# Performance work log

Measured on AMD Instinct MI355X. Metric: run time of the kernel, lower is better.

The kernel has to match this reference:

```python
import jax, jax.numpy as jnp
import numpy as np

B, C_IN, H, W = 4, 1536, 64, 64   # SGI input: cat of three 512-ch encoder maps at 64x64
HID, OUT = 1536, 512
N = H * W


def _grid_edge_index(h, w):
    # 4-connected bidirectional grid, matching SGI.grid_edge_index
    idx = np.arange(h * w).reshape(h, w)
    right = np.stack([idx[:, :-1].ravel(), idx[:, 1:].ravel()])
    down = np.stack([idx[:-1, :].ravel(), idx[1:, :].ravel()])
    ei = np.concatenate([right, down, right[::-1], down[::-1]], axis=1)
    return ei.astype(np.int32)


def setup_inputs() -> dict:
    key = jax.random.key(0)
    ks = jax.random.split(key, 7)
    ei = _grid_edge_index(H, W)
    s = 0.02
    return {
        "x":  jax.random.normal(ks[0], (B, C_IN, H, W), jnp.float32),
        "W1": jax.random.normal(ks[1], (C_IN, HID), jnp.float32) * s,
        "b1": jnp.zeros((HID,), jnp.float32),
        "W2": jax.random.normal(ks[2], (HID, OUT), jnp.float32) * s,
        "b2": jnp.zeros((OUT,), jnp.float32),
        "Wl": jax.random.normal(ks[3], (C_IN, OUT), jnp.float32) * s,
        "bl": jnp.zeros((OUT,), jnp.float32),
        "src": jnp.asarray(ei[0]),
        "dst": jnp.asarray(ei[1]),
    }


def _gcn(h_in, Wt, b, src, dst, inv_sqrt_deg, inv_deg):
    # PyG GCNConv: lin -> symmetric-normalized aggregation (with self loops) -> +bias
    h = h_in @ Wt                                   # [B, N, F]
    norm = inv_sqrt_deg[src] * inv_sqrt_deg[dst]    # [E]
    msgs = h[:, src, :] * norm[None, :, None]       # [B, E, F]
    # self-loop contribution has norm 1/deg_i
    agg = (h * inv_deg[None, :, None]).at[:, dst, :].add(msgs)
    return agg + b


def reference(x, W1, b1, W2, b2, Wl, bl, src, dst):
    Bb, C, Hh, Ww = x.shape
    n = Hh * Ww
    # degree including self loop (graph is symmetric)
    deg = jnp.zeros((n,), x.dtype).at[dst].add(1.0) + 1.0
    inv_sqrt_deg = jax.lax.rsqrt(deg)
    inv_deg = 1.0 / deg

    xt = x.reshape(Bb, C, n).transpose(0, 2, 1)     # [B, N, C]
    identity = xt
    origin = xt @ Wl + bl                           # [B, N, OUT]
    h = jax.nn.relu(_gcn(xt, W1, b1, src, dst, inv_sqrt_deg, inv_deg))
    h = _gcn(h + identity, W2, b2, src, dst, inv_sqrt_deg, inv_deg)
    out = h * origin                                # [B, N, OUT]
    return out.transpose(0, 2, 1).reshape(Bb, out.shape[-1], Hh, Ww)
```

## Files before the change

### kernel.cpp

```cpp
#include <hip/hip_runtime.h>
#include <hip/hip_bf16.h>
#include <stdint.h>


typedef __bf16 bf16;
typedef float f32x4 __attribute__((ext_vector_type(4)));
typedef bf16 bf16x8 __attribute__((ext_vector_type(8)));

#define NB 4
#define NN 4096
#define CIN 1536
#define HIDF 1536
#define OUTF 512

__device__ __forceinline__ float degree_of(int n) {
  const int x = n & 63, y = n >> 6;
  return 1.0f + (x > 0) + (x < 63) + (y > 0) + (y < 63);
}
__device__ __forceinline__ float deg2(int gx, int gy) {
  return 1.0f + (gx > 0) + (gx < 63) + (gy > 0) + (gy < 63);
}

#define XBLK 6144
#define W1BLK 576
#define W2BLK 192

__global__ __launch_bounds__(256) void prep(
    const float* __restrict__ x, const float* __restrict__ W1,
    const float* __restrict__ W2, const float* __restrict__ Wl,
    bf16* __restrict__ xt, bf16* __restrict__ xa, bf16* __restrict__ w1t,
    bf16* __restrict__ w2t, bf16* __restrict__ wlt) {
  __shared__ float vt[64 * 64];
  __shared__ float at[64 * 64];
  const int B = blockIdx.x, t = threadIdx.x;
  const int tx = t & 15, ty = t >> 4;
  const int lane = t & 63, w = t >> 6;
  const int u = lane & 7, n3 = lane >> 3;

  if (B < XBLK) {
    const int slot = B >> 3;
    const int nt = (B & 7) * 8 + (slot & 7);
    const int ct = (slot >> 3) % 24;
    const int bb = (slot >> 3) / 24;
    const int gy = nt;
    const int n0 = nt * 64, c0 = ct * 64;
    const float* xb = x + (long)bb * CIN * NN;
#pragma unroll
    for (int cc = 0; cc < 4; cc++) {
      const int cl = ty * 4 + cc;
      const float* row = xb + (long)(c0 + cl) * NN + n0;
      const int nb = tx * 4;
      f32x4 v = *(const f32x4*)(row + nb);
      f32x4 up = {0.f, 0.f, 0.f, 0.f};
      f32x4 dn = {0.f, 0.f, 0.f, 0.f};
      if (gy > 0) up = *(const f32x4*)(row + nb - 64);
      if (gy < 63) dn = *(const f32x4*)(row + nb + 64);
      const float lf = (tx > 0) ? row[nb - 1] : 0.f;
      const float rt = (tx < 15) ? row[nb + 4] : 0.f;
      f32x4 a;
#pragma unroll
      for (int i = 0; i < 4; i++) {
        const int gx = nb + i;
        const float degn = deg2(gx, gy);
        float s = v[i] * (1.0f / degn);
        const float lv = (i == 0) ? lf : v[i - 1];
        const float rv = (i == 3) ? rt : v[i + 1];
        if (gx > 0) s += lv * rsqrtf(degn * deg2(gx - 1, gy));
        if (gx < 63) s += rv * rsqrtf(degn * deg2(gx + 1, gy));
        if (gy > 0) s += up[i] * rsqrtf(degn * deg2(gx, gy - 1));
        if (gy < 63) s += dn[i] * rsqrtf(degn * deg2(gx, gy + 1));
        a[i] = s;
      }
      const int chunk = tx ^ (2 * ((cl >> 3) & 7));
      *(f32x4*)&vt[cl * 64 + chunk * 4] = v;
      *(f32x4*)&at[cl * 64 + chunk * 4] = a;
    }
    __syncthreads();
    bf16* xtb = xt + (long)bb * NN * CIN;
    bf16* xab = xa + (long)bb * NN * CIN;
#pragma unroll
    for (int q = 0; q < 4; q++) {
      const int j = q * 4 + w;
      const int arr = j & 1, r = j >> 1;
      const int nl = n3 + 8 * r;
      const float* s = arr ? at : vt;
      bf16x8 o;
#pragma unroll
      for (int jj = 0; jj < 8; jj++) {
        const int cl = u * 8 + jj;
        const int col = nl ^ (8 * ((cl >> 3) & 7));
        o[jj] = (bf16)s[cl * 64 + col];
      }
      bf16* outp = arr ? xab : xtb;
      *(bf16x8*)&outp[(long)(n0 + nl) * CIN + c0 + u * 8] = o;
    }
  } else {
    int B2 = B - XBLK;
    const float* srcp;
    bf16* dstp;
    int Fdim, Kd, nt, ct;
    if (B2 < W1BLK) {
      nt = B2 / 24; ct = B2 % 24; srcp = W1; dstp = w1t; Fdim = HIDF; Kd = CIN;
    } else if (B2 < W1BLK + W2BLK) {
      const int l = B2 - W1BLK;
      nt = l / 24; ct = l % 24; srcp = W2; dstp = w2t; Fdim = OUTF; Kd = HIDF;
    } else {
      const int l = B2 - W1BLK - W2BLK;
      nt = l / 24; ct = l % 24; srcp = Wl; dstp = wlt; Fdim = OUTF; Kd = CIN;
    }
    const int n0 = nt * 64, c0 = ct * 64;
#pragma unroll
    for (int cc = 0; cc < 4; cc++) {
      const int cl = ty * 4 + cc;
      const float* row = srcp + (long)(c0 + cl) * Fdim + n0;
      f32x4 v = *(const f32x4*)(row + tx * 4);
      const int chunk = tx ^ (2 * ((cl >> 3) & 7));
      *(f32x4*)&vt[cl * 64 + chunk * 4] = v;
    }
    __syncthreads();
#pragma unroll
    for (int q = 0; q < 2; q++) {
      const int r = q * 4 + w;
      const int nl = n3 + 8 * r;
      bf16x8 o;
#pragma unroll
      for (int jj = 0; jj < 8; jj++) {
        const int cl = u * 8 + jj;
        const int col = nl ^ (8 * ((cl >> 3) & 7));
        o[jj] = (bf16)vt[cl * 64 + col];
      }
      *(bf16x8*)&dstp[(long)(n0 + nl) * Kd + c0 + u * 8] = o;
    }
  }
}

__device__ __forceinline__ void async_copy16(const void* g, void* l) {
  __builtin_amdgcn_global_load_lds(
      (const __attribute__((address_space(1))) void*)g,
      (__attribute__((address_space(3))) void*)l, 16, 0, 0);
}

struct GemmCtx {
  f32x4 acc[4][4];
  int wave, lane, wm, wn, quad, l15;
};

__device__ __forceinline__ void gemm_init(GemmCtx& cx, int t) {
  cx.wave = t >> 6;
  cx.lane = t & 63;
  cx.wm = (cx.wave & 1) * 64;
  cx.wn = (cx.wave >> 1) * 64;
  cx.quad = cx.lane >> 4;
  cx.l15 = cx.lane & 15;
#pragma unroll
  for (int i = 0; i < 4; i++)
#pragma unroll
    for (int j = 0; j < 4; j++) cx.acc[i][j] = {0.f, 0.f, 0.f, 0.f};
}

template <int K>
__device__ __forceinline__ void gemm_kloop(GemmCtx& cx, const bf16* Ab,
                                           const bf16* Bb, bf16* As,
                                           bf16* Bs) {
  const int r = cx.lane >> 3, c8 = cx.lane & 7;
  const int fchunk = c8 ^ r;
  for (int kt = 0; kt < K; kt += 64) {
#pragma unroll
    for (int i = 0; i < 4; i++) {
      const int row = i * 32 + cx.wave * 8;
      async_copy16(Ab + (long)(row + r) * K + kt + fchunk * 8, &As[row * 64]);
      async_copy16(Bb + (long)(row + r) * K + kt + fchunk * 8, &Bs[row * 64]);
    }
    __syncthreads();
#pragma unroll
    for (int kk = 0; kk < 2; kk++) {
      const int q = kk * 4 + cx.quad;
      bf16x8 af[4], bfv[4];
#pragma unroll
      for (int mr = 0; mr < 4; mr++) {
        const int m = cx.wm + mr * 16 + cx.l15;
        af[mr] = *(const bf16x8*)&As[m * 64 + (q ^ (m & 7)) * 8];
      }
#pragma unroll
      for (int nc = 0; nc < 4; nc++) {
        const int n = cx.wn + nc * 16 + cx.l15;
        bfv[nc] = *(const bf16x8*)&Bs[n * 64 + (q ^ (n & 7)) * 8];
      }
#pragma unroll
      for (int mr = 0; mr < 4; mr++)
#pragma unroll
        for (int nc = 0; nc < 4; nc++)
          cx.acc[mr][nc] = __builtin_amdgcn_mfma_f32_16x16x32_bf16(
              af[mr], bfv[nc], cx.acc[mr][nc], 0, 0, 0);
    }
    __syncthreads();
  }
}

__global__ __launch_bounds__(256) void gemm_h(
    const bf16* __restrict__ xa, const bf16* __restrict__ w1t,
    const bf16* __restrict__ xt, bf16* __restrict__ h,
    const float* __restrict__ b1) {
  __shared__ bf16 As[128 * 64];
  __shared__ bf16 Bs[128 * 64];
  GemmCtx cx;
  gemm_init(cx, threadIdx.x);
  const int m0 = blockIdx.x * 128, n0 = blockIdx.y * 128, z = blockIdx.z;
  gemm_kloop<CIN>(cx, xa + (long)z * NN * CIN + (long)m0 * CIN,
                  w1t + (long)n0 * CIN, As, Bs);
  const bf16* Xb = xt + (long)z * NN * HIDF;
  bf16* Cb = h + (long)z * NN * HIDF;
#pragma unroll
  for (int mr = 0; mr < 4; mr++)
#pragma unroll
    for (int nc = 0; nc < 4; nc++) {
      const int gn = n0 + cx.wn + nc * 16 + cx.l15;
      const float bv = b1[gn];
#pragma unroll
      for (int j = 0; j < 4; j++) {
        const int gm = m0 + cx.wm + mr * 16 + cx.quad * 4 + j;
        float v = cx.acc[mr][nc][j] + bv;
        v = v > 0.f ? v : 0.f;
        Cb[(long)gm * HIDF + gn] = (bf16)(v + (float)Xb[(long)gm * HIDF + gn]);
      }
    }
}

template <bool ADD_BIAS>
__global__ __launch_bounds__(256) void gemm_f32(
    const bf16* __restrict__ A, const bf16* __restrict__ Bw,
    float* __restrict__ C, const float* __restrict__ bias) {
  __shared__ bf16 As[128 * 64];
  __shared__ bf16 Bs[128 * 64];
  GemmCtx cx;
  gemm_init(cx, threadIdx.x);
  const int m0 = blockIdx.x * 128, n0 = blockIdx.y * 128, z = blockIdx.z;
  gemm_kloop<CIN>(cx, A + (long)z * NN * CIN + (long)m0 * CIN,
                  Bw + (long)n0 * CIN, As, Bs);
  float* Cb = C + (long)z * NN * OUTF;
#pragma unroll
  for (int mr = 0; mr < 4; mr++)
#pragma unroll
    for (int nc = 0; nc < 4; nc++) {
      const int gn = n0 + cx.wn + nc * 16 + cx.l15;
      float bv = 0.f;
      if (ADD_BIAS) bv = bias[gn];
#pragma unroll
      for (int j = 0; j < 4; j++) {
        const int gm = m0 + cx.wm + mr * 16 + cx.quad * 4 + j;
        Cb[(long)gm * OUTF + gn] = cx.acc[mr][nc][j] + bv;
      }
    }
}

__global__ __launch_bounds__(256) void stencil2(
    const float* __restrict__ G2, const float* __restrict__ Orig,
    const float* __restrict__ b2, float* __restrict__ out) {
  __shared__ float tile[16][513];
  const int blk = blockIdx.x;
  const int s = ((blk & 7) << 5) + (blk >> 3);
  const int n0 = s * 16, b = blockIdx.y;
  const int t = threadIdx.x;
  const int fq = t & 127, nl = t >> 7;
  const int f = fq * 4;
  const f32x4 bv = *(const f32x4*)(b2 + f);
#pragma unroll
  for (int p = 0; p < 8; p++) {
    const int nLoc = p * 2 + nl;
    const int n = n0 + nLoc;
    const int gx = n & 63, gy = n >> 6;
    const float degn = degree_of(n);
    const float ws = 1.0f / degn;
    const long rb = ((long)b * NN + n) * (long)OUTF + f;
    f32x4 g = *(const f32x4*)(G2 + rb);
    f32x4 a;
#pragma unroll
    for (int i = 0; i < 4; i++) a[i] = g[i] * ws;
    if (gx > 0) {
      const float w = rsqrtf(degn * degree_of(n - 1));
      f32x4 u = *(const f32x4*)(G2 + rb - OUTF);
#pragma unroll
      for (int i = 0; i < 4; i++) a[i] += u[i] * w;
    }
    if (gx < 63) {
      const float w = rsqrtf(degn * degree_of(n + 1));
      f32x4 u = *(const f32x4*)(G2 + rb + OUTF);
#pragma unroll
      for (int i = 0; i < 4; i++) a[i] += u[i] * w;
    }
    if (gy > 0) {
      const float w = rsqrtf(degn * degree_of(n - 64));
      f32x4 u = *(const f32x4*)(G2 + rb - 64L * OUTF);
#pragma unroll
      for (int i = 0; i < 4; i++) a[i] += u[i] * w;
    }
    if (gy < 63) {
      const float w = rsqrtf(degn * degree_of(n + 64));
      f32x4 u = *(const f32x4*)(G2 + rb + 64L * OUTF);
#pragma unroll
      for (int i = 0; i < 4; i++) a[i] += u[i] * w;
    }
    f32x4 og = *(const f32x4*)(Orig + rb);
#pragma unroll
    for (int i = 0; i < 4; i++) tile[nLoc][f + i] = (a[i] + bv[i]) * og[i];
  }
  __syncthreads();
  const int nl2 = t & 15, f0 = t >> 4;
#pragma unroll
  for (int q = 0; q < 32; q++) {
    const int ff = q * 16 + f0;
    out[((long)b * OUTF + ff) * (long)NN + n0 + nl2] = tile[nl2][ff];
  }
}

extern "C" void kernel_launch(void* const* d_in, const int* in_sizes, int n_in,
                              void* d_out, int out_size, void* d_ws,
                              size_t ws_size, hipStream_t stream) {
  const float* x = (const float*)d_in[0];
  const float* W1 = (const float*)d_in[1];
  const float* b1 = (const float*)d_in[2];
  const float* W2 = (const float*)d_in[3];
  const float* b2 = (const float*)d_in[4];
  const float* Wl = (const float*)d_in[5];
  const float* bl = (const float*)d_in[6];
  float* out = (float*)d_out;

  uint8_t* ws = (uint8_t*)d_ws;
  size_t off = 0;
  auto alloc = [&](size_t bytes) -> void* {
    void* p = ws + off;
    off += (bytes + 255) & ~(size_t)255;
    return p;
  };
  bf16* xt = (bf16*)alloc((size_t)NB * NN * CIN * 2);
  bf16* xa = (bf16*)alloc((size_t)NB * NN * CIN * 2);
  bf16* hb = (bf16*)alloc((size_t)NB * NN * HIDF * 2);
  bf16* w1t = (bf16*)alloc((size_t)HIDF * CIN * 2);
  bf16* w2t = (bf16*)alloc((size_t)OUTF * HIDF * 2);
  bf16* wlt = (bf16*)alloc((size_t)OUTF * CIN * 2);
  float* origin = (float*)xa;
  float* g2 = (float*)xt;

  prep<<<XBLK + W1BLK + 2 * W2BLK, 256, 0, stream>>>(x, W1, W2, Wl, xt, xa,
                                                     w1t, w2t, wlt);
  gemm_h<<<dim3(NN / 128, HIDF / 128, NB), 256, 0, stream>>>(xa, w1t, xt, hb,
                                                             b1);
  gemm_f32<true><<<dim3(NN / 128, OUTF / 128, NB), 256, 0, stream>>>(
      xt, wlt, origin, bl);
  gemm_f32<false><<<dim3(NN / 128, OUTF / 128, NB), 256, 0, stream>>>(
      hb, w2t, g2, nullptr);
  stencil2<<<dim3(256, NB), 256, 0, stream>>>(g2, origin, b2, out);
}
```

Baseline: 372.3 us.

## Merge layer-1 and origin GEMMs into one launch, split-K the second GEMM

Combines the hidden-layer GEMM and the origin projection GEMM into a single grid so both run concurrently and fill the device better. The second GEMM (512 outputs) is split along K into two halves written to separate buffers, doubling its block count, and the stencil sums both partials. The residual add of the input tile is staged through shared memory for coalesced loads. This costs an extra fp32 buffer for origin and extra stencil reads of the second partial, with a fallback path when workspace is too small.

```diff
diff --git a/kernel.cpp b/kernel.cpp
--- a/kernel.cpp
+++ b/kernel.cpp
@@ -12,6 +12,7 @@
 #define CIN 1536
 #define HIDF 1536
 #define OUTF 512
+#define YH (HIDF / 128)
 
 __device__ __forceinline__ float degree_of(int n) {
   const int x = n & 63, y = n >> 6;
@@ -158,18 +159,18 @@
     for (int j = 0; j < 4; j++) cx.acc[i][j] = {0.f, 0.f, 0.f, 0.f};
 }
 
-template <int K>
+template <int LDK>
 __device__ __forceinline__ void gemm_kloop(GemmCtx& cx, const bf16* Ab,
-                                           const bf16* Bb, bf16* As,
-                                           bf16* Bs) {
+                                           const bf16* Bb, bf16* As, bf16* Bs,
+                                           int k0, int k1) {
   const int r = cx.lane >> 3, c8 = cx.lane & 7;
   const int fchunk = c8 ^ r;
-  for (int kt = 0; kt < K; kt += 64) {
+  for (int kt = k0; kt < k1; kt += 64) {
 #pragma unroll
     for (int i = 0; i < 4; i++) {
       const int row = i * 32 + cx.wave * 8;
-      async_copy16(Ab + (long)(row + r) * K + kt + fchunk * 8, &As[row * 64]);
-      async_copy16(Bb + (long)(row + r) * K + kt + fchunk * 8, &Bs[row * 64]);
+      async_copy16(Ab + (long)(row + r) * LDK + kt + fchunk * 8, &As[row * 64]);
+      async_copy16(Bb + (long)(row + r) * LDK + kt + fchunk * 8, &Bs[row * 64]);
     }
     __syncthreads();
 #pragma unroll
@@ -197,65 +198,98 @@
   }
 }
 
-__global__ __launch_bounds__(256) void gemm_h(
-    const bf16* __restrict__ xa, const bf16* __restrict__ w1t,
-    const bf16* __restrict__ xt, bf16* __restrict__ h,
-    const float* __restrict__ b1) {
-  __shared__ bf16 As[128 * 64];
-  __shared__ bf16 Bs[128 * 64];
+__global__ __launch_bounds__(256) void gemm_ho(
+    const bf16* __restrict__ xa, const bf16* __restrict__ xt,
+    const bf16* __restrict__ w1t, const bf16* __restrict__ wlt,
+    bf16* __restrict__ h, float* __restrict__ orig,
+    const float* __restrict__ b1, const float* __restrict__ bl, int y_off) {
+  __shared__ bf16 S[2 * 128 * 64];
+  bf16* As = S;
+  bf16* Bs = S + 128 * 64;
   GemmCtx cx;
   gemm_init(cx, threadIdx.x);
-  const int m0 = blockIdx.x * 128, n0 = blockIdx.y * 128, z = blockIdx.z;
-  gemm_kloop<CIN>(cx, xa + (long)z * NN * CIN + (long)m0 * CIN,
-                  w1t + (long)n0 * CIN, As, Bs);
-  const bf16* Xb = xt + (long)z * NN * HIDF;
-  bf16* Cb = h + (long)z * NN * HIDF;
+  const int yb = blockIdx.y + y_off;
+  const int m0 = blockIdx.x * 128, z = blockIdx.z;
+  const bool is_h = yb < YH;
+  const int n0 = (is_h ? yb : yb - YH) * 128;
+  const bf16* A = (is_h ? xa : xt) + (long)z * NN * CIN + (long)m0 * CIN;
+  const bf16* Bw = (is_h ? w1t : wlt) + (long)n0 * CIN;
+  gemm_kloop<CIN>(cx, A, Bw, As, Bs, 0, CIN);
+
+  if (is_h) {
+    const bf16* Xb = xt + (long)z * NN * CIN;
+    bf16* Xs = S;
+    const int lane = cx.lane, wave = cx.wave;
+#pragma unroll
+    for (int i = 0; i < 8; i++) {
+      const int rb = i * 16 + wave * 4;
+      async_copy16(
+          Xb + (long)(m0 + rb + (lane >> 4)) * CIN + n0 + (lane & 15) * 8,
+          &Xs[rb * 128]);
+    }
+    __syncthreads();
+    bf16* Cb = h + (long)z * NN * HIDF;
+#pragma unroll
+    for (int mr = 0; mr < 4; mr++)
+#pragma unroll
+      for (int nc = 0; nc < 4; nc++) {
+        const int gnl = cx.wn + nc * 16 + cx.l15;
+        const float bv = b1[n0 + gnl];
+#pragma unroll
+        for (int j = 0; j < 4; j++) {
+          const int gml = cx.wm + mr * 16 + cx.quad * 4 + j;
+          float v = cx.acc[mr][nc][j] + bv;
+          v = v > 0.f ? v : 0.f;
+          v += (float)Xs[gml * 128 + gnl];
+          Cb[(long)(m0 + gml) * HIDF + n0 + gnl] = (bf16)v;
+        }
+      }
+  } else {
+    float* Cb = orig + (long)z * NN * OUTF;
+#pragma unroll
+    for (int mr = 0; mr < 4; mr++)
+#pragma unroll
+      for (int nc = 0; nc < 4; nc++) {
+        const int gn = n0 + cx.wn + nc * 16 + cx.l15;
+        const float bv = bl[gn];
+#pragma unroll
+        for (int j = 0; j < 4; j++) {
+          const int gm = m0 + cx.wm + mr * 16 + cx.quad * 4 + j;
+          Cb[(long)gm * OUTF + gn] = cx.acc[mr][nc][j] + bv;
+        }
+      }
+  }
+}
+
+__global__ __launch_bounds__(256) void gemm2k(
+    const bf16* __restrict__ hb, const bf16* __restrict__ w2t,
+    float* __restrict__ g2a, float* __restrict__ g2b, int kspan) {
+  __shared__ bf16 S[2 * 128 * 64];
+  GemmCtx cx;
+  gemm_init(cx, threadIdx.x);
+  const int m0 = blockIdx.x * 128, n0 = blockIdx.y * 128;
+  const int z = blockIdx.z & 3, part = blockIdx.z >> 2;
+  const int k0 = part * kspan;
+  gemm_kloop<HIDF>(cx, hb + (long)z * NN * HIDF + (long)m0 * HIDF,
+                   w2t + (long)n0 * HIDF, S, S + 128 * 64, k0, k0 + kspan);
+  float* Cb = (part ? g2b : g2a) + (long)z * NN * OUTF;
 #pragma unroll
   for (int mr = 0; mr < 4; mr++)
 #pragma unroll
     for (int nc = 0; nc < 4; nc++) {
       const int gn = n0 + cx.wn + nc * 16 + cx.l15;
-      const float bv = b1[gn];
 #pragma unroll
       for (int j = 0; j < 4; j++) {
         const int gm = m0 + cx.wm + mr * 16 + cx.quad * 4 + j;
-        float v = cx.acc[mr][nc][j] + bv;
-        v = v > 0.f ? v : 0.f;
-        Cb[(long)gm * HIDF + gn] = (bf16)(v + (float)Xb[(long)gm * HIDF + gn]);
-      }
-    }
-}
-
-template <bool ADD_BIAS>
-__global__ __launch_bounds__(256) void gemm_f32(
-    const bf16* __restrict__ A, const bf16* __restrict__ Bw,
-    float* __restrict__ C, const float* __restrict__ bias) {
-  __shared__ bf16 As[128 * 64];
-  __shared__ bf16 Bs[128 * 64];
-  GemmCtx cx;
-  gemm_init(cx, threadIdx.x);
-  const int m0 = blockIdx.x * 128, n0 = blockIdx.y * 128, z = blockIdx.z;
-  gemm_kloop<CIN>(cx, A + (long)z * NN * CIN + (long)m0 * CIN,
-                  Bw + (long)n0 * CIN, As, Bs);
-  float* Cb = C + (long)z * NN * OUTF;
-#pragma unroll
-  for (int mr = 0; mr < 4; mr++)
-#pragma unroll
-    for (int nc = 0; nc < 4; nc++) {
-      const int gn = n0 + cx.wn + nc * 16 + cx.l15;
-      float bv = 0.f;
-      if (ADD_BIAS) bv = bias[gn];
-#pragma unroll
-      for (int j = 0; j < 4; j++) {
-        const int gm = m0 + cx.wm + mr * 16 + cx.quad * 4 + j;
-        Cb[(long)gm * OUTF + gn] = cx.acc[mr][nc][j] + bv;
+        Cb[(long)gm * OUTF + gn] = cx.acc[mr][nc][j];
       }
     }
 }
 
 __global__ __launch_bounds__(256) void stencil2(
-    const float* __restrict__ G2, const float* __restrict__ Orig,
-    const float* __restrict__ b2, float* __restrict__ out) {
+    const float* __restrict__ g2a, const float* __restrict__ g2b,
+    const float* __restrict__ Orig, const float* __restrict__ b2,
+    float* __restrict__ out, int two) {
   __shared__ float tile[16][513];
   const int blk = blockIdx.x;
   const int s = ((blk & 7) << 5) + (blk >> 3);
@@ -271,34 +305,37 @@
     const int gx = n & 63, gy = n >> 6;
     const float degn = degree_of(n);
     const float ws = 1.0f / degn;
+    const float wL = (gx > 0) ? rsqrtf(degn * degree_of(n - 1)) : 0.f;
+    const float wR = (gx < 63) ? rsqrtf(degn * degree_of(n + 1)) : 0.f;
+    const float wU = (gy > 0) ? rsqrtf(degn * degree_of(n - 64)) : 0.f;
+    const float wD = (gy < 63) ? rsqrtf(degn * degree_of(n + 64)) : 0.f;
     const long rb = ((long)b * NN + n) * (long)OUTF + f;
-    f32x4 g = *(const f32x4*)(G2 + rb);
-    f32x4 a;
-#pragma unroll
-    for (int i = 0; i < 4; i++) a[i] = g[i] * ws;
-    if (gx > 0) {
-      const float w = rsqrtf(degn * degree_of(n - 1));
-      f32x4 u = *(const f32x4*)(G2 + rb - OUTF);
-#pragma unroll
-      for (int i = 0; i < 4; i++) a[i] += u[i] * w;
-    }
-    if (gx < 63) {
-      const float w = rsqrtf(degn * degree_of(n + 1));
-      f32x4 u = *(const f32x4*)(G2 + rb + OUTF);
-#pragma unroll
-      for (int i = 0; i < 4; i++) a[i] += u[i] * w;
-    }
-    if (gy > 0) {
-      const float w = rsqrtf(degn * degree_of(n - 64));
-      f32x4 u = *(const f32x4*)(G2 + rb - 64L * OUTF);
-#pragma unroll
-      for (int i = 0; i < 4; i++) a[i] += u[i] * w;
-    }
-    if (gy < 63) {
-      const float w = rsqrtf(degn * degree_of(n + 64));
-      f32x4 u = *(const f32x4*)(G2 + rb + 64L * OUTF);
-#pragma unroll
-      for (int i = 0; i < 4; i++) a[i] += u[i] * w;
+    f32x4 a = {0.f, 0.f, 0.f, 0.f};
+    for (int q = 0; q <= two; q++) {
+      const float* G = q ? g2b : g2a;
+      f32x4 g = *(const f32x4*)(G + rb);
+#pragma unroll
+      for (int i = 0; i < 4; i++) a[i] += g[i] * ws;
+      if (gx > 0) {
+        f32x4 u = *(const f32x4*)(G + rb - OUTF);
+#pragma unroll
+        for (int i = 0; i < 4; i++) a[i] += u[i] * wL;
+      }
+      if (gx < 63) {
+        f32x4 u = *(const f32x4*)(G + rb + OUTF);
+#pragma unroll
+        for (int i = 0; i < 4; i++) a[i] += u[i] * wR;
+      }
+      if (gy > 0) {
+        f32x4 u = *(const f32x4*)(G + rb - 64L * OUTF);
+#pragma unroll
+        for (int i = 0; i < 4; i++) a[i] += u[i] * wU;
+      }
+      if (gy < 63) {
+        f32x4 u = *(const f32x4*)(G + rb + 64L * OUTF);
+#pragma unroll
+        for (int i = 0; i < 4; i++) a[i] += u[i] * wD;
+      }
     }
     f32x4 og = *(const f32x4*)(Orig + rb);
 #pragma unroll
@@ -338,16 +375,27 @@
   bf16* w1t = (bf16*)alloc((size_t)HIDF * CIN * 2);
   bf16* w2t = (bf16*)alloc((size_t)OUTF * HIDF * 2);
   bf16* wlt = (bf16*)alloc((size_t)OUTF * CIN * 2);
-  float* origin = (float*)xa;
-  float* g2 = (float*)xt;
+  const size_t obytes = (size_t)NB * NN * OUTF * 4;
+  const bool merged = (ws_size >= off + obytes);
+  float* origin = merged ? (float*)alloc(obytes) : (float*)xa;
+  float* g2a = merged ? (float*)xa : (float*)xt;
+  float* g2b = (float*)xt;
 
   prep<<<XBLK + W1BLK + 2 * W2BLK, 256, 0, stream>>>(x, W1, W2, Wl, xt, xa,
                                                      w1t, w2t, wlt);
-  gemm_h<<<dim3(NN / 128, HIDF / 128, NB), 256, 0, stream>>>(xa, w1t, xt, hb,
-                                                             b1);
-  gemm_f32<true><<<dim3(NN / 128, OUTF / 128, NB), 256, 0, stream>>>(
-      xt, wlt, origin, bl);
-  gemm_f32<false><<<dim3(NN / 128, OUTF / 128, NB), 256, 0, stream>>>(
-      hb, w2t, g2, nullptr);
-  stencil2<<<dim3(256, NB), 256, 0, stream>>>(g2, origin, b2, out);
-}
+  if (merged) {
+    gemm_ho<<<dim3(NN / 128, YH + OUTF / 128, NB), 256, 0, stream>>>(
+        xa, xt, w1t, wlt, hb, origin, b1, bl, 0);
+    gemm2k<<<dim3(NN / 128, OUTF / 128, NB * 2), 256, 0, stream>>>(
+        hb, w2t, g2a, g2b, CIN / 2);
+    stencil2<<<dim3(256, NB), 256, 0, stream>>>(g2a, g2b, origin, b2, out, 1);
+  } else {
+    gemm_ho<<<dim3(NN / 128, YH, NB), 256, 0, stream>>>(xa, xt, w1t, wlt, hb,
+                                                        origin, b1, bl, 0);
+    gemm_ho<<<dim3(NN / 128, OUTF / 128, NB), 256, 0, stream>>>(
+        xa, xt, w1t, wlt, hb, origin, b1, bl, YH);
+    gemm2k<<<dim3(NN / 128, OUTF / 128, NB), 256, 0, stream>>>(hb, w2t, g2a,
+                                                               g2a, CIN);
+    stencil2<<<dim3(256, NB), 256, 0, stream>>>(g2a, g2a, origin, b2, out, 0);
+  }
+}
```

After: 387.5 us. 4.1% more time.
